# Kernel optimization log

Measured on AMD Instinct MI355X. Metric: run time of the kernel, lower is better.

The kernel has to match this reference:

```python
import jax, jax.numpy as jnp
import numpy as np

B, K, E = 8192, 16, 64          # subgraphs, nodes/subgraph, edges/subgraph
FIN, FOUT = 300, 64
ALPHA, BETA = 1.0, 0.6
EPS = 1e-12


def _l2n(x):
    # F.normalize(x, p=2, dim=-1)
    return x / jnp.maximum(jnp.linalg.norm(x, axis=-1, keepdims=True), EPS)


def _flat(idx):
    # local node ids -> global ids in the batched graph (offset b*K)
    return (idx + (jnp.arange(B, dtype=idx.dtype) * K)[:, None]).ravel()


def _spmm(src_f, dst_f, w, x):
    # h[dst] += w * x[src]  over all B*E edges; x: [B,K,F]
    F = x.shape[-1]
    xf = x.reshape(B * K, F)
    msg = xf[src_f] * w.ravel()[:, None]
    return jnp.zeros((B * K, F), x.dtype).at[dst_f].add(msg).reshape(B, K, F)


def _deg_inv_sqrt(idx_f):
    d = jnp.zeros((B * K,), jnp.float32).at[idx_f].add(1.0)
    return jnp.clip(d, 1.0) ** -0.5


def _enc(feat, src, dst, w, W, b):
    # OneLayerGCNWithGlobalAdg: zero anchor feat, GraphConv(norm='none', edge_weight), ReLU
    anchor_out = jax.nn.relu(feat[:, 0, :] @ W + b)          # [B,FOUT]
    fz = feat.at[:, 0, :].set(0.0)
    x = fz @ W                                               # [B,K,FOUT]
    h = jax.nn.relu(_spmm(_flat(src), _flat(dst), w, x) + b)
    pool = h.mean(axis=1)                                    # mean over all K nodes
    return _l2n(h), _l2n(pool), _l2n(anchor_out)


def _dec(h, src, dst, w, W, b):
    # OneLayerGCN: GraphConv(norm='both', edge_weight), ReLU
    sf, df = _flat(src), _flat(dst)
    nsrc = _deg_inv_sqrt(sf).reshape(B, K, 1)   # out-degree^-1/2
    ndst = _deg_inv_sqrt(df).reshape(B, K, 1)   # in-degree^-1/2
    x = (h * nsrc) @ W                          # project first (FOUT < FIN)
    hd = jax.nn.relu(_spmm(sf, df, w, x) * ndst + b)
    pool = hd[:, :-1, :].mean(axis=1)           # mean over nodes [:-1]
    anchor = hd[:, 0, :]
    return _l2n(hd), _l2n(pool), _l2n(anchor)


def setup_inputs() -> dict:
    key = jax.random.key(0)
    ks = jax.random.split(key, 16)
    g_enc = float(np.sqrt(6.0 / (FIN + FOUT)))
    g_dec = float(np.sqrt(6.0 / (FOUT + FIN)))
    g_bil = float(np.sqrt(6.0 / (FOUT + FOUT)))
    inp = {
        'feat_p1': jax.random.normal(ks[0], (B, K, FIN), jnp.float32),
        'feat_p2': jax.random.normal(ks[1], (B, K, FIN), jnp.float32),
        'feat_n':  jax.random.normal(ks[2], (B, K, FIN), jnp.float32),
        'w_p1': jax.random.uniform(ks[3], (B, E), jnp.float32),
        'w_p2': jax.random.uniform(ks[4], (B, E), jnp.float32),
        'w_n':  jax.random.uniform(ks[5], (B, E), jnp.float32),
        'W_enc': jax.random.uniform(ks[6], (FIN, FOUT), jnp.float32, -g_enc, g_enc),
        'b_enc': jnp.zeros((FOUT,), jnp.float32),
        'W_dec': jax.random.uniform(ks[7], (FOUT, FIN), jnp.float32, -g_dec, g_dec),
        'b_dec': jnp.zeros((FIN,), jnp.float32),
        'W_bil': jax.random.uniform(ks[8], (FOUT, FOUT), jnp.float32, -g_bil, g_bil),
        'b_bil': jnp.zeros((1,), jnp.float32),
        'src_p1': jax.random.randint(ks[9], (B, E), 0, K, jnp.int32),
        'dst_p1': jax.random.randint(ks[10], (B, E), 0, K, jnp.int32),
        'src_p2': jax.random.randint(ks[11], (B, E), 0, K, jnp.int32),
        'dst_p2': jax.random.randint(ks[12], (B, E), 0, K, jnp.int32),
        'src_n':  jax.random.randint(ks[13], (B, E), 0, K, jnp.int32),
        'dst_n':  jax.random.randint(ks[14], (B, E), 0, K, jnp.int32),
    }
    return inp


def reference(feat_p1, feat_p2, feat_n, w_p1, w_p2, w_n,
              W_enc, b_enc, W_dec, b_dec, W_bil, b_bil,
              src_p1, dst_p1, src_p2, dst_p2, src_n, dst_n):
    ori1 = feat_p1[:, 0, :]
    ori2 = feat_p2[:, 0, :]

    h1, pool1, a1 = _enc(feat_p1, src_p1, dst_p1, w_p1, W_enc, b_enc)
    h2, pool2, a2 = _enc(feat_p2, src_p2, dst_p2, w_p2, W_enc, b_enc)
    _, pooln, _ = _enc(feat_n, src_n, dst_n, w_n, W_enc, b_enc)

    def disc(r, a):  # nn.Bilinear(FOUT, FOUT, 1)
        return jnp.einsum('bj,jk,bk->b', r, W_bil, a)[:, None] + b_bil

    ps1 = jax.nn.sigmoid(disc(pool1, a1))
    ps2 = jax.nn.sigmoid(disc(pool2, a2))
    ns1 = jax.nn.sigmoid(disc(pooln, a1))
    ns2 = jax.nn.sigmoid(disc(pooln, a2))

    _, _, da1 = _dec(h1, src_p1, dst_p1, w_p1, W_dec, b_dec)
    _, _, da2 = _dec(h2, src_p2, dst_p2, w_p2, W_dec, b_dec)

    m1 = jnp.mean(jnp.log(ps1) + jnp.log(1.0 - ns1))
    m2 = jnp.mean(jnp.log(ps2) + jnp.log(1.0 - ns2))
    L_con = -((m1 / 2 + m2 / 2) / 2)
    L_gen = (jnp.mean(jnp.square(da1 - ori1)) + jnp.mean(jnp.square(da2 - ori2))) / 2
    L = ALPHA * L_con + BETA * L_gen

    attributes_num = jnp.sqrt(jnp.float32(FIN))
    contr = (ns1 - ps1 + 1.0) / 2 + (ns2 - ps2 + 1.0) / 2          # [B,1]
    gen = (jnp.linalg.norm(da1 - ori1) / attributes_num / 2
           + jnp.linalg.norm(da2 - ori2) / attributes_num / 2)      # scalar
    single_predict_scores = ALPHA * contr + BETA * gen
    return L, single_predict_scores
```

## Files before the change

### kernel.cpp

```cpp
#include <hip/hip_runtime.h>

#define BB 8192
#define KK 16
#define EE 64
#define FINN 300

typedef __attribute__((ext_vector_type(8))) short short8;
typedef __attribute__((ext_vector_type(4))) float f32x4;

__device__ __forceinline__ unsigned packbf(float a, float b) {
  unsigned ua = __float_as_uint(a), ub = __float_as_uint(b);
  ua = (ua + 0x7fffu + ((ua >> 16) & 1u)) >> 16;
  ub = (ub + 0x7fffu + ((ub >> 16) & 1u)) >> 16;
  return ua | (ub << 16);
}
__device__ __forceinline__ float redC(float v) {
  v += __shfl_xor(v, 1); v += __shfl_xor(v, 2);
  v += __shfl_xor(v, 4); v += __shfl_xor(v, 8);
  return v;
}
__device__ __forceinline__ float redQ(float v) {
  v += __shfl_xor(v, 16); v += __shfl_xor(v, 32);
  return v;
}
__device__ __forceinline__ float waveSum(float v) {
#pragma unroll
  for (int off = 32; off; off >>= 1) v += __shfl_xor(v, off);
  return v;
}
__device__ __forceinline__ double waveSumD(double v) {
#pragma unroll
  for (int off = 32; off; off >>= 1) v += __shfl_xor(v, off);
  return v;
}
__device__ __forceinline__ float logsig(float z) {
  return fminf(z, 0.f) - log1pf(expf(-fabsf(z)));
}

__global__ void prep_kernel(const float* __restrict__ Wenc, uint4* __restrict__ wB) {
  const int id = blockIdx.x * 256 + threadIdx.x;
  if (id >= 2560) return;
  const int lane = id & 63;
  const int step = (id >> 6) % 10;
  const int nt = id / 640;
  const int n = nt * 16 + (lane & 15);
  const int kb = step * 32 + (lane >> 4) * 8;
  float f[8];
#pragma unroll
  for (int j2 = 0; j2 < 8; ++j2) {
    const int k = kb + j2;
    f[j2] = (k < FINN) ? Wenc[k * 64 + n] : 0.f;
  }
  uint4 o;
  o.x = packbf(f[0], f[1]); o.y = packbf(f[2], f[3]);
  o.z = packbf(f[4], f[5]); o.w = packbf(f[6], f[7]);
  wB[id] = o;
}

__global__ __launch_bounds__(256, 4) void enc_kernel(
    const float* __restrict__ fpn, const float* __restrict__ fp1, const float* __restrict__ fp2,
    const float* __restrict__ wn, const float* __restrict__ w1, const float* __restrict__ w2,
    const int* __restrict__ sn, const int* __restrict__ s1, const int* __restrict__ s2,
    const int* __restrict__ dn, const int* __restrict__ d1, const int* __restrict__ d2,
    const uint4* __restrict__ wB, const float* __restrict__ benc,
    float* __restrict__ pooln, float* __restrict__ pool1, float* __restrict__ pool2,
    float* __restrict__ a1o, float* __restrict__ a2o,
    float* __restrict__ g1o, float* __restrict__ g2o,
    float* __restrict__ nd1o, float* __restrict__ nd2o)
{
  __shared__ char smem[40960];
  unsigned* featU = (unsigned*)smem;
  char* xBc = smem;
  float* AdjL = (float*)(smem + 16384);
  char* AdjBc = smem + 20480;
  float* coefL = (float*)(smem + 24576);
  float* xAnch = (float*)(smem + 24832);

  const int tid = threadIdx.x, lane = tid & 63, wv = tid >> 6;
  const int q = lane >> 4, c = lane & 15;
  const int kf = blockIdx.x >> 11;
  const int bg = blockIdx.x & 2047;
  const int b0 = bg * 4;

  const float* feat; const float* wedg; const int* src; const int* dst;
  float* pool_out; float* a_out; float* g_out; float* nd0_out;
  if (kf == 0) {
    feat = fpn; wedg = wn; src = sn; dst = dn;
    pool_out = pooln; a_out = nullptr; g_out = nullptr; nd0_out = nullptr;
  } else if (kf == 1) {
    feat = fp1; wedg = w1; src = s1; dst = d1;
    pool_out = pool1; a_out = a1o; g_out = g1o; nd0_out = nd1o;
  } else {
    feat = fp2; wedg = w2; src = s2; dst = d2;
    pool_out = pool2; a_out = a2o; g_out = g2o; nd0_out = nd2o;
  }

  uint4 bfr[10];
  {
    const uint4* p = wB + (wv * 10) * 64 + lane;
#pragma unroll
    for (int s = 0; s < 10; ++s) bfr[s] = p[s * 64];
  }
  {
    const float4* gf = (const float4*)(feat + (size_t)b0 * (KK * FINN));
    for (int it = tid; it < 4800; it += 256) {
      const float4 v = gf[it];
      const int row = it / 75, c4 = it - row * 75;
      uint2 o;
      o.x = packbf(v.x, v.y);
      o.y = packbf(v.z, v.w);
      *(uint2*)&featU[row * 160 + ((c4 * 2) ^ ((row & 7) << 2))] = o;
    }
    for (int it = tid; it < 640; it += 256) {
      const int row = it / 10, dlog = 150 + (it - row * 10);
      featU[row * 160 + (dlog ^ ((row & 7) << 2))] = 0;
    }
  }
  __syncthreads();

  f32x4 acc[4];
#pragma unroll
  for (int m = 0; m < 4; ++m) acc[m] = (f32x4){0.f, 0.f, 0.f, 0.f};
  const int xr = (c & 7) << 4;
#pragma unroll
  for (int s = 0; s < 10; ++s) {
    const short8 b8 = *(const short8*)&bfr[s];
#pragma unroll
    for (int m = 0; m < 4; ++m) {
      const short8 a8 = *(const short8*)(smem + (m * 16 + c) * 640 + ((s * 64 + q * 16) ^ xr));
      acc[m] = __builtin_amdgcn_mfma_f32_16x16x32_bf16(a8, b8, acc[m], 0, 0, 0);
    }
  }
  __syncthreads();

#pragma unroll
  for (int m = 0; m < 4; ++m) {
    unsigned* dp = (unsigned*)(xBc + ((m * 4 + wv) * 64 + (q >> 1) * 16 + c) * 16 + (q & 1) * 8);
    dp[0] = packbf(acc[m][0], acc[m][1]);
    dp[1] = packbf(acc[m][2], acc[m][3]);
    if (q == 0) xAnch[m * 64 + wv * 16 + c] = acc[m][0];
  }
  {
    const uint4 z = {0, 0, 0, 0};
    for (int i = tid; i < 512; i += 256)
      ((uint4*)xBc)[(i >> 5) * 64 + 32 + (i & 31)] = z;
    for (int i = tid; i < 512; i += 256)
      ((uint4*)(smem + 16384))[i] = z;
  }
  __syncthreads();

  const int g = wv;
  const int bu = b0 + wv;
  const int se = src[bu * EE + lane];
  const int de = dst[bu * EE + lane];
  const float we = wedg[bu * EE + lane];

  float dinv_reg = 0.f;
#pragma unroll
  for (int k = 0; k < KK; ++k) {
    const int cnt = __popcll(__ballot(se == k));
    if (lane == k) dinv_reg = rsqrtf(fmaxf((float)cnt, 1.f));
  }
  if (nd0_out) {
    const int cd0 = __popcll(__ballot(de == 0));
    if (lane == 0) nd0_out[bu] = rsqrtf(fmaxf((float)cd0, 1.f));
  }
  atomicAdd(&AdjL[g * 256 + de * 16 + se], we);
  __threadfence_block();
  {
    const f32x4 v = *(const f32x4*)(AdjL + g * 256 + lane * 4);
    const float v0 = ((lane & 3) == 0) ? 0.f : v[0];
    unsigned* w = (unsigned*)(AdjBc + g * 1024 + (lane >> 2) * 64 + (lane & 3) * 8);
    w[0] = packbf(v0, v[1]);
    w[1] = packbf(v[2], v[3]);
  }
  if (g_out && lane < KK)
    coefL[g * 16 + lane] = AdjL[g * 256 + lane] * dinv_reg;
  __threadfence_block();

  const short8 aAdj = *(const short8*)(AdjBc + g * 1024 + c * 64 + q * 16);
  float bj[4], h[4][4];
#pragma unroll
  for (int nt = 0; nt < 4; ++nt) bj[nt] = benc[nt * 16 + c];
#pragma unroll
  for (int nt = 0; nt < 4; ++nt) {
    const short8 xb = *(const short8*)(xBc + ((g * 4 + nt) * 64 + lane) * 16);
    f32x4 cc = (f32x4){0.f, 0.f, 0.f, 0.f};
    cc = __builtin_amdgcn_mfma_f32_16x16x32_bf16(aAdj, xb, cc, 0, 0, 0);
#pragma unroll
    for (int r = 0; r < 4; ++r) h[nt][r] = fmaxf(cc[r] + bj[nt], 0.f);
  }

  float pl[4];
#pragma unroll
  for (int nt = 0; nt < 4; ++nt)
    pl[nt] = redQ(h[nt][0] + h[nt][1] + h[nt][2] + h[nt][3]);
  float pn2 = redC(pl[0] * pl[0] + pl[1] * pl[1] + pl[2] * pl[2] + pl[3] * pl[3]);
  const float pinv = 1.f / fmaxf(sqrtf(pn2), 1e-12f);
  if (q == 0)
#pragma unroll
    for (int nt = 0; nt < 4; ++nt)
      pool_out[(size_t)bu * 64 + nt * 16 + c] = pl[nt] * pinv;

  if (g_out) {
    float rnv[4];
#pragma unroll
    for (int r = 0; r < 4; ++r) {
      float s2 = redC(h[0][r] * h[0][r] + h[1][r] * h[1][r] +
                      h[2][r] * h[2][r] + h[3][r] * h[3][r]);
      rnv[r] = 1.f / fmaxf(sqrtf(s2), 1e-12f);
    }
    float gp[4] = {0.f, 0.f, 0.f, 0.f};
#pragma unroll
    for (int r = 0; r < 4; ++r) {
      const float cf = coefL[g * 16 + q * 4 + r] * rnv[r];
#pragma unroll
      for (int nt = 0; nt < 4; ++nt) gp[nt] = fmaf(cf, h[nt][r], gp[nt]);
    }
#pragma unroll
    for (int nt = 0; nt < 4; ++nt) gp[nt] = redQ(gp[nt]);
    if (q == 1)
#pragma unroll
      for (int nt = 0; nt < 4; ++nt)
        g_out[(size_t)bu * 64 + nt * 16 + c] = gp[nt];
  }
  if (a_out) {
    float av[4], an2 = 0.f;
#pragma unroll
    for (int nt = 0; nt < 4; ++nt) {
      av[nt] = fmaxf(xAnch[g * 64 + nt * 16 + c] + bj[nt], 0.f);
      an2 += av[nt] * av[nt];
    }
    an2 = redC(an2);
    const float ainv = 1.f / fmaxf(sqrtf(an2), 1e-12f);
    if (q == 2)
#pragma unroll
      for (int nt = 0; nt < 4; ++nt)
        a_out[(size_t)bu * 64 + nt * 16 + c] = av[nt] * ainv;
  }
}

__global__ __launch_bounds__(256) void dec_kernel(
    const float* __restrict__ g1b, const float* __restrict__ g2b,
    const float* __restrict__ nd1b, const float* __restrict__ nd2b,
    const float* __restrict__ Wdec, const float* __restrict__ bdec,
    const float* __restrict__ feat1, const float* __restrict__ feat2,
    float* __restrict__ dArr1, float* __restrict__ dArr2)
{
  __shared__ float red[16];
  __shared__ float invA_s, invB_s;
  const int t = threadIdx.x, b = blockIdx.x;
  const float gva = g1b[(size_t)b * 64 + (t & 63)];
  const float gvb = g2b[(size_t)b * 64 + (t & 63)];
  const float nda = nd1b[b], ndb = nd2b[b];
  const int f0 = t, f1 = t + 256;
  const bool has1 = (f1 < FINN);
  float ya0 = 0.f, ya1 = 0.f, yb0 = 0.f, yb1 = 0.f;
  for (int jj = 0; jj < 64; ++jj) {
    const float w0 = Wdec[jj * FINN + f0];
    const float ga = __shfl(gva, jj), gb = __shfl(gvb, jj);
    ya0 = fmaf(ga, w0, ya0);
    yb0 = fmaf(gb, w0, yb0);
    if (has1) {
      const float w1 = Wdec[jj * FINN + f1];
      ya1 = fmaf(ga, w1, ya1);
      yb1 = fmaf(gb, w1, yb1);
    }
  }
  const float bd0 = bdec[f0];
  const float bd1 = has1 ? bdec[f1] : 0.f;
  const float aa0 = fmaxf(ya0 * nda + bd0, 0.f);
  const float aa1 = has1 ? fmaxf(ya1 * nda + bd1, 0.f) : 0.f;
  const float ab0 = fmaxf(yb0 * ndb + bd0, 0.f);
  const float ab1 = has1 ? fmaxf(yb1 * ndb + bd1, 0.f) : 0.f;
  float sA = waveSum(aa0 * aa0 + aa1 * aa1);
  float sB = waveSum(ab0 * ab0 + ab1 * ab1);
  if ((t & 63) == 0) { red[t >> 6] = sA; red[8 + (t >> 6)] = sB; }
  __syncthreads();
  if (t == 0) {
    invA_s = 1.f / fmaxf(sqrtf(red[0] + red[1] + red[2] + red[3]), 1e-12f);
    invB_s = 1.f / fmaxf(sqrtf(red[8] + red[9] + red[10] + red[11]), 1e-12f);
  }
  __syncthreads();
  const float invA = invA_s, invB = invB_s;
  const float* __restrict__ ori1 = feat1 + (size_t)b * KK * FINN;
  const float* __restrict__ ori2 = feat2 + (size_t)b * KK * FINN;
  const float dA0 = aa0 * invA - ori1[f0];
  const float dA1 = has1 ? (aa1 * invA - ori1[f1]) : 0.f;
  const float dB0 = ab0 * invB - ori2[f0];
  const float dB1 = has1 ? (ab1 * invB - ori2[f1]) : 0.f;
  float sdA = waveSum(dA0 * dA0 + dA1 * dA1);
  float sdB = waveSum(dB0 * dB0 + dB1 * dB1);
  if ((t & 63) == 0) { red[t >> 6] = sdA; red[8 + (t >> 6)] = sdB; }
  __syncthreads();
  if (t == 0) {
    dArr1[b] = red[0] + red[1] + red[2] + red[3];
    dArr2[b] = red[8] + red[9] + red[10] + red[11];
  }
}

__global__ __launch_bounds__(256) void bil_kernel(
    const float* __restrict__ pool1, const float* __restrict__ pool2,
    const float* __restrict__ pooln, const float* __restrict__ a1b,
    const float* __restrict__ a2b, const float* __restrict__ Wbil,
    const float* __restrict__ bbil, float* __restrict__ contr,
    float* __restrict__ tArr1, float* __restrict__ tArr2)
{
  const int tid = threadIdx.x, wv = tid >> 6, j = tid & 63;
  const int bu = blockIdx.x * 4 + wv;
  const float p1 = pool1[(size_t)bu * 64 + j];
  const float p2 = pool2[(size_t)bu * 64 + j];
  const float pn = pooln[(size_t)bu * 64 + j];
  const float A1 = a1b[(size_t)bu * 64 + j];
  const float A2 = a2b[(size_t)bu * 64 + j];
  float v1 = 0.f, v2 = 0.f, vn = 0.f;
  for (int jj = 0; jj < 64; ++jj) {
    const float wr = Wbil[jj * 64 + j];
    v1 = fmaf(__shfl(p1, jj), wr, v1);
    v2 = fmaf(__shfl(p2, jj), wr, v2);
    vn = fmaf(__shfl(pn, jj), wr, vn);
  }
  const float d11 = waveSum(v1 * A1);
  const float d22 = waveSum(v2 * A2);
  const float dn1 = waveSum(vn * A1);
  const float dn2 = waveSum(vn * A2);
  if (j == 0) {
    const float bb = bbil[0];
    const float z11 = d11 + bb, z22 = d22 + bb, zn1 = dn1 + bb, zn2 = dn2 + bb;
    const float ps1 = 1.f / (1.f + expf(-z11));
    const float ps2 = 1.f / (1.f + expf(-z22));
    const float ns1 = 1.f / (1.f + expf(-zn1));
    const float ns2 = 1.f / (1.f + expf(-zn2));
    contr[bu] = (ns1 - ps1 + 1.f) * 0.5f + (ns2 - ps2 + 1.f) * 0.5f;
    tArr1[bu] = logsig(z11) + logsig(-zn1);
    tArr2[bu] = logsig(z22) + logsig(-zn2);
  }
}

__global__ __launch_bounds__(1024) void redfin_kernel(const float* __restrict__ parts,
                                                      float* __restrict__ genw,
                                                      float* __restrict__ out)
{
  __shared__ double sred[16];
  const int t = threadIdx.x, lane = t & 63, wv = t >> 6;
  const int seg = t >> 8;
  const float* __restrict__ p = parts + (size_t)seg * BB;
  double s = 0.0;
  for (int i = (t & 255); i < BB; i += 256) s += (double)p[i];
  s = waveSumD(s);
  if (lane == 0) sred[wv] = s;
  __syncthreads();
  if (t == 0) {
    const double T1 = sred[0] + sred[1] + sred[2] + sred[3];
    const double T2 = sred[4] + sred[5] + sred[6] + sred[7];
    const double S1d = sred[8] + sred[9] + sred[10] + sred[11];
    const double S2d = sred[12] + sred[13] + sred[14] + sred[15];
    const double m1 = S1d / (double)BB, m2 = S2d / (double)BB;
    const double Lcon = -(m1 + m2) * 0.25;
    const double Lgen = (T1 + T2) / (2.0 * (double)BB * (double)FINN);
    out[0] = (float)(Lcon + 0.6 * Lgen);
    genw[0] = (float)((sqrt(T1) + sqrt(T2)) / (2.0 * sqrt((double)FINN)));
  }
}

__global__ void score_kernel(const float* __restrict__ contr, const float* __restrict__ genw,
                             float* __restrict__ out)
{
  const int i = blockIdx.x * blockDim.x + threadIdx.x;
  if (i < BB) out[1 + i] = fmaf(0.6f, genw[0], contr[i]);
}

extern "C" void kernel_launch(void* const* d_in, const int* in_sizes, int n_in,
                              void* d_out, int out_size, void* d_ws, size_t ws_size,
                              hipStream_t stream)
{
  const float* feat_p1 = (const float*)d_in[0];
  const float* feat_p2 = (const float*)d_in[1];
  const float* feat_n  = (const float*)d_in[2];
  const float* w_p1 = (const float*)d_in[3];
  const float* w_p2 = (const float*)d_in[4];
  const float* w_n  = (const float*)d_in[5];
  const float* W_enc = (const float*)d_in[6];
  const float* b_enc = (const float*)d_in[7];
  const float* W_dec = (const float*)d_in[8];
  const float* b_dec = (const float*)d_in[9];
  const float* W_bil = (const float*)d_in[10];
  const float* b_bil = (const float*)d_in[11];
  const int* src_p1 = (const int*)d_in[12];
  const int* dst_p1 = (const int*)d_in[13];
  const int* src_p2 = (const int*)d_in[14];
  const int* dst_p2 = (const int*)d_in[15];
  const int* src_n  = (const int*)d_in[16];
  const int* dst_n  = (const int*)d_in[17];
  float* out = (float*)d_out;

  float* genw = (float*)((char*)d_ws + 32);
  uint4* wsB = (uint4*)((char*)d_ws + 1024);
  float* fws = (float*)((char*)d_ws + 49152);
  float* pool1 = fws;
  float* pool2 = pool1 + (size_t)BB * 64;
  float* pooln = pool2 + (size_t)BB * 64;
  float* a1 = pooln + (size_t)BB * 64;
  float* a2 = a1 + (size_t)BB * 64;
  float* g1 = a2 + (size_t)BB * 64;
  float* g2 = g1 + (size_t)BB * 64;
  float* nd01 = g2 + (size_t)BB * 64;
  float* nd02 = nd01 + BB;
  float* contr = nd02 + BB;
  float* parts = contr + BB;
  float* dArr1 = parts;
  float* dArr2 = parts + BB;
  float* tArr1 = parts + 2 * BB;
  float* tArr2 = parts + 3 * BB;

  hipLaunchKernelGGL(prep_kernel, dim3(10), dim3(256), 0, stream, W_enc, wsB);
  hipLaunchKernelGGL(enc_kernel, dim3(3 * BB / 4), dim3(256), 0, stream,
                     feat_n, feat_p1, feat_p2,
                     w_n, w_p1, w_p2,
                     src_n, src_p1, src_p2,
                     dst_n, dst_p1, dst_p2,
                     wsB, b_enc,
                     pooln, pool1, pool2,
                     a1, a2, g1, g2, nd01, nd02);
  hipLaunchKernelGGL(dec_kernel, dim3(BB), dim3(256), 0, stream,
                     g1, g2, nd01, nd02, W_dec, b_dec, feat_p1, feat_p2, dArr1, dArr2);
  hipLaunchKernelGGL(bil_kernel, dim3(BB / 4), dim3(256), 0, stream,
                     pool1, pool2, pooln, a1, a2, W_bil, b_bil, contr, tArr1, tArr2);
  hipLaunchKernelGGL(redfin_kernel, dim3(1), dim3(1024), 0, stream, parts, genw, out);
  hipLaunchKernelGGL(score_kernel, dim3((BB + 255) / 256), dim3(256), 0, stream,
                     contr, genw, out);
}
```

Measured before the change: 584.7 us.

## Halve encoder LDS via two-phase feature staging, batch decoder per 4 graphs

The encoder now stages the 64-row feature tile in two halves of 32 rows, running the MFMA for each half in turn. This cuts the shared buffer from 40960 to 25856 bytes and raises the launch-bounds occupancy hint from 4 to 6, at the cost of an extra barrier and serialised load/compute phases. The decoder handles 4 subgraphs per block, so each W_dec load is reused across 4 graphs and the launch uses a quarter as many blocks. The final reduction is split into 4 parallel blocks with the loss computation folded into the score kernel. bf16 packing now uses the native conversion instead of manual rounding.

```diff
diff --git a/kernel.cpp b/kernel.cpp
--- a/kernel.cpp
+++ b/kernel.cpp
@@ -8,11 +8,11 @@
 typedef __attribute__((ext_vector_type(8))) short short8;
 typedef __attribute__((ext_vector_type(4))) float f32x4;
 
+__device__ __forceinline__ unsigned short bf16r(float x) {
+  return __builtin_bit_cast(unsigned short, (__bf16)x);
+}
 __device__ __forceinline__ unsigned packbf(float a, float b) {
-  unsigned ua = __float_as_uint(a), ub = __float_as_uint(b);
-  ua = (ua + 0x7fffu + ((ua >> 16) & 1u)) >> 16;
-  ub = (ub + 0x7fffu + ((ub >> 16) & 1u)) >> 16;
-  return ua | (ub << 16);
+  return (unsigned)bf16r(a) | ((unsigned)bf16r(b) << 16);
 }
 __device__ __forceinline__ float redC(float v) {
   v += __shfl_xor(v, 1); v += __shfl_xor(v, 2);
@@ -57,7 +57,7 @@
   wB[id] = o;
 }
 
-__global__ __launch_bounds__(256, 4) void enc_kernel(
+__global__ __launch_bounds__(256, 6) void enc_kernel(
     const float* __restrict__ fpn, const float* __restrict__ fp1, const float* __restrict__ fp2,
     const float* __restrict__ wn, const float* __restrict__ w1, const float* __restrict__ w2,
     const int* __restrict__ sn, const int* __restrict__ s1, const int* __restrict__ s2,
@@ -68,7 +68,7 @@
     float* __restrict__ g1o, float* __restrict__ g2o,
     float* __restrict__ nd1o, float* __restrict__ nd2o)
 {
-  __shared__ char smem[40960];
+  __shared__ char smem[25856];
   unsigned* featU = (unsigned*)smem;
   char* xBc = smem;
   float* AdjL = (float*)(smem + 16384);
@@ -101,20 +101,19 @@
 #pragma unroll
     for (int s = 0; s < 10; ++s) bfr[s] = p[s * 64];
   }
-  {
-    const float4* gf = (const float4*)(feat + (size_t)b0 * (KK * FINN));
-    for (int it = tid; it < 4800; it += 256) {
-      const float4 v = gf[it];
-      const int row = it / 75, c4 = it - row * 75;
-      uint2 o;
-      o.x = packbf(v.x, v.y);
-      o.y = packbf(v.z, v.w);
-      *(uint2*)&featU[row * 160 + ((c4 * 2) ^ ((row & 7) << 2))] = o;
-    }
-    for (int it = tid; it < 640; it += 256) {
-      const int row = it / 10, dlog = 150 + (it - row * 10);
-      featU[row * 160 + (dlog ^ ((row & 7) << 2))] = 0;
-    }
+  const float4* gf = (const float4*)(feat + (size_t)b0 * (KK * FINN));
+
+  for (int it = tid; it < 2400; it += 256) {
+    const float4 v = gf[it];
+    const int row = it / 75, c4 = it - row * 75;
+    uint2 o;
+    o.x = packbf(v.x, v.y);
+    o.y = packbf(v.z, v.w);
+    *(uint2*)&featU[row * 160 + ((c4 * 2) ^ ((row & 7) << 2))] = o;
+  }
+  for (int it = tid; it < 320; it += 256) {
+    const int row = it / 10, dlog = 150 + (it - row * 10);
+    featU[row * 160 + (dlog ^ ((row & 7) << 2))] = 0;
   }
   __syncthreads();
 
@@ -122,12 +121,34 @@
 #pragma unroll
   for (int m = 0; m < 4; ++m) acc[m] = (f32x4){0.f, 0.f, 0.f, 0.f};
   const int xr = (c & 7) << 4;
+
 #pragma unroll
   for (int s = 0; s < 10; ++s) {
     const short8 b8 = *(const short8*)&bfr[s];
 #pragma unroll
-    for (int m = 0; m < 4; ++m) {
+    for (int m = 0; m < 2; ++m) {
       const short8 a8 = *(const short8*)(smem + (m * 16 + c) * 640 + ((s * 64 + q * 16) ^ xr));
+      acc[m] = __builtin_amdgcn_mfma_f32_16x16x32_bf16(a8, b8, acc[m], 0, 0, 0);
+    }
+  }
+  __syncthreads();
+
+  for (int it = tid; it < 2400; it += 256) {
+    const float4 v = gf[2400 + it];
+    const int row = it / 75, c4 = it - row * 75;
+    uint2 o;
+    o.x = packbf(v.x, v.y);
+    o.y = packbf(v.z, v.w);
+    *(uint2*)&featU[row * 160 + ((c4 * 2) ^ ((row & 7) << 2))] = o;
+  }
+  __syncthreads();
+
+#pragma unroll
+  for (int s = 0; s < 10; ++s) {
+    const short8 b8 = *(const short8*)&bfr[s];
+#pragma unroll
+    for (int m = 2; m < 4; ++m) {
+      const short8 a8 = *(const short8*)(smem + ((m - 2) * 16 + c) * 640 + ((s * 64 + q * 16) ^ xr));
       acc[m] = __builtin_amdgcn_mfma_f32_16x16x32_bf16(a8, b8, acc[m], 0, 0, 0);
     }
   }
@@ -247,56 +268,71 @@
     const float* __restrict__ feat1, const float* __restrict__ feat2,
     float* __restrict__ dArr1, float* __restrict__ dArr2)
 {
-  __shared__ float red[16];
-  __shared__ float invA_s, invB_s;
-  const int t = threadIdx.x, b = blockIdx.x;
-  const float gva = g1b[(size_t)b * 64 + (t & 63)];
-  const float gvb = g2b[(size_t)b * 64 + (t & 63)];
-  const float nda = nd1b[b], ndb = nd2b[b];
+  __shared__ float red[4][8];
+  __shared__ float invs[8];
+  const int t = threadIdx.x, lane = t & 63, wv = t >> 6;
+  const int b0 = blockIdx.x * 4;
+  float gva[4], gvb[4], nda[4], ndb[4];
+#pragma unroll
+  for (int gg = 0; gg < 4; ++gg) {
+    gva[gg] = g1b[(size_t)(b0 + gg) * 64 + lane];
+    gvb[gg] = g2b[(size_t)(b0 + gg) * 64 + lane];
+    nda[gg] = nd1b[b0 + gg];
+    ndb[gg] = nd2b[b0 + gg];
+  }
   const int f0 = t, f1 = t + 256;
   const bool has1 = (f1 < FINN);
-  float ya0 = 0.f, ya1 = 0.f, yb0 = 0.f, yb1 = 0.f;
+  float yA0[4] = {0.f, 0.f, 0.f, 0.f}, yA1[4] = {0.f, 0.f, 0.f, 0.f};
+  float yB0[4] = {0.f, 0.f, 0.f, 0.f}, yB1[4] = {0.f, 0.f, 0.f, 0.f};
   for (int jj = 0; jj < 64; ++jj) {
     const float w0 = Wdec[jj * FINN + f0];
-    const float ga = __shfl(gva, jj), gb = __shfl(gvb, jj);
-    ya0 = fmaf(ga, w0, ya0);
-    yb0 = fmaf(gb, w0, yb0);
-    if (has1) {
-      const float w1 = Wdec[jj * FINN + f1];
-      ya1 = fmaf(ga, w1, ya1);
-      yb1 = fmaf(gb, w1, yb1);
+    const float w1 = has1 ? Wdec[jj * FINN + f1] : 0.f;
+#pragma unroll
+    for (int gg = 0; gg < 4; ++gg) {
+      const float ga = __shfl(gva[gg], jj);
+      const float gb = __shfl(gvb[gg], jj);
+      yA0[gg] = fmaf(ga, w0, yA0[gg]);
+      yA1[gg] = fmaf(ga, w1, yA1[gg]);
+      yB0[gg] = fmaf(gb, w0, yB0[gg]);
+      yB1[gg] = fmaf(gb, w1, yB1[gg]);
     }
   }
   const float bd0 = bdec[f0];
   const float bd1 = has1 ? bdec[f1] : 0.f;
-  const float aa0 = fmaxf(ya0 * nda + bd0, 0.f);
-  const float aa1 = has1 ? fmaxf(ya1 * nda + bd1, 0.f) : 0.f;
-  const float ab0 = fmaxf(yb0 * ndb + bd0, 0.f);
-  const float ab1 = has1 ? fmaxf(yb1 * ndb + bd1, 0.f) : 0.f;
-  float sA = waveSum(aa0 * aa0 + aa1 * aa1);
-  float sB = waveSum(ab0 * ab0 + ab1 * ab1);
-  if ((t & 63) == 0) { red[t >> 6] = sA; red[8 + (t >> 6)] = sB; }
-  __syncthreads();
-  if (t == 0) {
-    invA_s = 1.f / fmaxf(sqrtf(red[0] + red[1] + red[2] + red[3]), 1e-12f);
-    invB_s = 1.f / fmaxf(sqrtf(red[8] + red[9] + red[10] + red[11]), 1e-12f);
-  }
-  __syncthreads();
-  const float invA = invA_s, invB = invB_s;
-  const float* __restrict__ ori1 = feat1 + (size_t)b * KK * FINN;
-  const float* __restrict__ ori2 = feat2 + (size_t)b * KK * FINN;
-  const float dA0 = aa0 * invA - ori1[f0];
-  const float dA1 = has1 ? (aa1 * invA - ori1[f1]) : 0.f;
-  const float dB0 = ab0 * invB - ori2[f0];
-  const float dB1 = has1 ? (ab1 * invB - ori2[f1]) : 0.f;
-  float sdA = waveSum(dA0 * dA0 + dA1 * dA1);
-  float sdB = waveSum(dB0 * dB0 + dB1 * dB1);
-  if ((t & 63) == 0) { red[t >> 6] = sdA; red[8 + (t >> 6)] = sdB; }
-  __syncthreads();
-  if (t == 0) {
-    dArr1[b] = red[0] + red[1] + red[2] + red[3];
-    dArr2[b] = red[8] + red[9] + red[10] + red[11];
-  }
+  float aa0[4], aa1[4], ab0[4], ab1[4];
+#pragma unroll
+  for (int gg = 0; gg < 4; ++gg) {
+    aa0[gg] = fmaxf(yA0[gg] * nda[gg] + bd0, 0.f);
+    aa1[gg] = has1 ? fmaxf(yA1[gg] * nda[gg] + bd1, 0.f) : 0.f;
+    ab0[gg] = fmaxf(yB0[gg] * ndb[gg] + bd0, 0.f);
+    ab1[gg] = has1 ? fmaxf(yB1[gg] * ndb[gg] + bd1, 0.f) : 0.f;
+    const float sA = waveSum(aa0[gg] * aa0[gg] + aa1[gg] * aa1[gg]);
+    const float sB = waveSum(ab0[gg] * ab0[gg] + ab1[gg] * ab1[gg]);
+    if (lane == 0) { red[wv][gg] = sA; red[wv][4 + gg] = sB; }
+  }
+  __syncthreads();
+  if (t < 8) invs[t] = 1.f / fmaxf(sqrtf(red[0][t] + red[1][t] + red[2][t] + red[3][t]), 1e-12f);
+  __syncthreads();
+  float sdA[4], sdB[4];
+#pragma unroll
+  for (int gg = 0; gg < 4; ++gg) {
+    const float* __restrict__ ori1 = feat1 + (size_t)(b0 + gg) * KK * FINN;
+    const float* __restrict__ ori2 = feat2 + (size_t)(b0 + gg) * KK * FINN;
+    const float dA0 = aa0[gg] * invs[gg] - ori1[f0];
+    const float dA1 = has1 ? (aa1[gg] * invs[gg] - ori1[f1]) : 0.f;
+    const float dB0 = ab0[gg] * invs[4 + gg] - ori2[f0];
+    const float dB1 = has1 ? (ab1[gg] * invs[4 + gg] - ori2[f1]) : 0.f;
+    sdA[gg] = waveSum(dA0 * dA0 + dA1 * dA1);
+    sdB[gg] = waveSum(dB0 * dB0 + dB1 * dB1);
+  }
+  __syncthreads();
+  if (lane == 0) {
+#pragma unroll
+    for (int gg = 0; gg < 4; ++gg) { red[wv][gg] = sdA[gg]; red[wv][4 + gg] = sdB[gg]; }
+  }
+  __syncthreads();
+  if (t < 4) dArr1[b0 + t] = red[0][t] + red[1][t] + red[2][t] + red[3][t];
+  else if (t < 8) dArr2[b0 + t - 4] = red[0][t] + red[1][t] + red[2][t] + red[3][t];
 }
 
 __global__ __launch_bounds__(256) void bil_kernel(
@@ -337,37 +373,33 @@
   }
 }
 
-__global__ __launch_bounds__(1024) void redfin_kernel(const float* __restrict__ parts,
-                                                      float* __restrict__ genw,
-                                                      float* __restrict__ out)
-{
-  __shared__ double sred[16];
+__global__ __launch_bounds__(256) void reduce_kernel(const float* __restrict__ parts,
+                                                     double* __restrict__ accs)
+{
+  __shared__ double sred[4];
   const int t = threadIdx.x, lane = t & 63, wv = t >> 6;
-  const int seg = t >> 8;
-  const float* __restrict__ p = parts + (size_t)seg * BB;
+  const float* __restrict__ p = parts + (size_t)blockIdx.x * BB;
   double s = 0.0;
-  for (int i = (t & 255); i < BB; i += 256) s += (double)p[i];
+  for (int i = t; i < BB; i += 256) s += (double)p[i];
   s = waveSumD(s);
   if (lane == 0) sred[wv] = s;
   __syncthreads();
-  if (t == 0) {
-    const double T1 = sred[0] + sred[1] + sred[2] + sred[3];
-    const double T2 = sred[4] + sred[5] + sred[6] + sred[7];
-    const double S1d = sred[8] + sred[9] + sred[10] + sred[11];
-    const double S2d = sred[12] + sred[13] + sred[14] + sred[15];
+  if (t == 0) accs[blockIdx.x] = sred[0] + sred[1] + sred[2] + sred[3];
+}
+
+__global__ void score_kernel(const double* __restrict__ accs,
+                             const float* __restrict__ contr, float* __restrict__ out)
+{
+  const int i = blockIdx.x * blockDim.x + threadIdx.x;
+  const double T1 = accs[0], T2 = accs[1], S1d = accs[2], S2d = accs[3];
+  if (i == 0) {
     const double m1 = S1d / (double)BB, m2 = S2d / (double)BB;
     const double Lcon = -(m1 + m2) * 0.25;
     const double Lgen = (T1 + T2) / (2.0 * (double)BB * (double)FINN);
     out[0] = (float)(Lcon + 0.6 * Lgen);
-    genw[0] = (float)((sqrt(T1) + sqrt(T2)) / (2.0 * sqrt((double)FINN)));
-  }
-}
-
-__global__ void score_kernel(const float* __restrict__ contr, const float* __restrict__ genw,
-                             float* __restrict__ out)
-{
-  const int i = blockIdx.x * blockDim.x + threadIdx.x;
-  if (i < BB) out[1 + i] = fmaf(0.6f, genw[0], contr[i]);
+  }
+  const float genw = (float)((sqrt(T1) + sqrt(T2)) / (2.0 * sqrt((double)FINN)));
+  if (i < BB) out[1 + i] = fmaf(0.6f, genw, contr[i]);
 }
 
 extern "C" void kernel_launch(void* const* d_in, const int* in_sizes, int n_in,
@@ -394,7 +426,7 @@
   const int* dst_n  = (const int*)d_in[17];
   float* out = (float*)d_out;
 
-  float* genw = (float*)((char*)d_ws + 32);
+  double* accs = (double*)d_ws;
   uint4* wsB = (uint4*)((char*)d_ws + 1024);
   float* fws = (float*)((char*)d_ws + 49152);
   float* pool1 = fws;
@@ -422,11 +454,11 @@
                      wsB, b_enc,
                      pooln, pool1, pool2,
                      a1, a2, g1, g2, nd01, nd02);
-  hipLaunchKernelGGL(dec_kernel, dim3(BB), dim3(256), 0, stream,
+  hipLaunchKernelGGL(dec_kernel, dim3(BB / 4), dim3(256), 0, stream,
                      g1, g2, nd01, nd02, W_dec, b_dec, feat_p1, feat_p2, dArr1, dArr2);
   hipLaunchKernelGGL(bil_kernel, dim3(BB / 4), dim3(256), 0, stream,
                      pool1, pool2, pooln, a1, a2, W_bil, b_bil, contr, tArr1, tArr2);
-  hipLaunchKernelGGL(redfin_kernel, dim3(1), dim3(1024), 0, stream, parts, genw, out);
+  hipLaunchKernelGGL(reduce_kernel, dim3(4), dim3(256), 0, stream, parts, accs);
   hipLaunchKernelGGL(score_kernel, dim3((BB + 255) / 256), dim3(256), 0, stream,
-                     contr, genw, out);
-}
+                     accs, contr, out);
+}
```

Result: faster. 559.0 us (-4.4%).
